# Kernel optimization log

Measured on AMD Instinct MI355X. Metric: run time of the kernel, lower is better.

## Reference

```python
import jax, jax.numpy as jnp
import numpy as np

D = 512
H = 8
FFN_H = 2048
NEG = -1.0e10


def layer_norm(x, gamma, beta, eps=1e-5):
    mu = jnp.mean(x, axis=-1, keepdims=True)
    var = jnp.var(x, axis=-1, keepdims=True)
    return (x - mu) * jax.lax.rsqrt(var + eps) * gamma + beta


def mha(x_q, x_kv, Wq, Wk, Wv, Wo, valid_lens):
    # x_q: [B,Tq,D], x_kv: [B,Tk,D]; valid_lens: [B,Tq] or [B]
    B, Tq, _ = x_q.shape
    Tk = x_kv.shape[1]
    dh = D // H
    q = (x_q @ Wq.T).reshape(B, Tq, H, dh).transpose(0, 2, 1, 3)  # [B,H,Tq,dh]
    k = (x_kv @ Wk.T).reshape(B, Tk, H, dh).transpose(0, 2, 1, 3)
    v = (x_kv @ Wv.T).reshape(B, Tk, H, dh).transpose(0, 2, 1, 3)
    scores = jnp.einsum('bhqd,bhkd->bhqk', q, k) / jnp.sqrt(jnp.float32(dh))
    pos = jnp.arange(Tk)
    if valid_lens.ndim == 1:  # [B] -> mask [B,1,1,Tk]
        mask = pos[None, None, None, :] < valid_lens[:, None, None, None]
    else:  # [B,Tq] -> mask [B,1,Tq,Tk]
        mask = pos[None, None, None, :] < valid_lens[:, None, :, None]
    scores = jnp.where(mask, scores, NEG)
    attn = jax.nn.softmax(scores, axis=-1)
    out = jnp.einsum('bhqk,bhkd->bhqd', attn, v)  # [B,H,Tq,dh]
    out = out.transpose(0, 2, 1, 3).reshape(B, Tq, D)
    return out @ Wo.T


def setup_inputs() -> dict:
    key = jax.random.key(0)
    ks = jax.random.split(key, 20)
    B, T = 32, 512
    s = 1.0 / np.sqrt(D)
    inp = {
        'X': jax.random.normal(ks[0], (B, T, D), jnp.float32),
        'enc_outputs': jax.random.normal(ks[1], (B, T, D), jnp.float32),
        'dec_valid_lens': jax.random.randint(ks[2], (B, T), 1, T + 1, jnp.int32),
        'enc_valid_lens': jax.random.randint(ks[3], (B,), 1, T + 1, jnp.int32),
    }
    names = ['Wq1', 'Wk1', 'Wv1', 'Wo1', 'Wq2', 'Wk2', 'Wv2', 'Wo2']
    for i, n in enumerate(names):
        inp[n] = jax.random.normal(ks[4 + i], (D, D), jnp.float32) * s
    inp['W1'] = jax.random.normal(ks[12], (FFN_H, D), jnp.float32) * s
    inp['b1'] = jnp.zeros((FFN_H,), jnp.float32)
    inp['W2'] = jax.random.normal(ks[13], (D, FFN_H), jnp.float32) * (1.0 / np.sqrt(FFN_H))
    inp['b2'] = jnp.zeros((D,), jnp.float32)
    for j in (1, 2, 3):
        inp[f'g{j}'] = jnp.ones((D,), jnp.float32)
        inp[f'be{j}'] = jnp.zeros((D,), jnp.float32)
    return inp


def reference(X, enc_outputs, dec_valid_lens, enc_valid_lens,
              Wq1, Wk1, Wv1, Wo1, Wq2, Wk2, Wv2, Wo2,
              W1, b1, W2, b2, g1, be1, g2, be2, g3, be3):
    # Training path: state[2][i] is None -> key_values = X. Dropout in eval mode (identity).
    X2 = mha(X, X, Wq1, Wk1, Wv1, Wo1, dec_valid_lens)            # self-attention
    Y = layer_norm(X + X2, g1, be1)                               # AddNorm1
    Y2 = mha(Y, enc_outputs, Wq2, Wk2, Wv2, Wo2, enc_valid_lens)  # cross-attention
    Z = layer_norm(Y + Y2, g2, be2)                               # AddNorm2
    F = (jax.nn.leaky_relu(Z @ W1.T + b1, 0.01)) @ W2.T + b2      # FFN (LeakyReLU slope 0.01)
    return layer_norm(Z + F, g3, be3)                             # AddNorm3
```

## Files before the change

kernel.cpp:

```cpp
#include <hip/hip_runtime.h>
#include <cstdint>
#include <cstddef>

typedef __bf16 bf16;
typedef __bf16 bf16x8 __attribute__((ext_vector_type(8)));
typedef float  f32x4  __attribute__((ext_vector_type(4)));
typedef unsigned short u16;

#define MD ((size_t)8388608)

__device__ __forceinline__ void async_copy16(const bf16* gp, bf16* lp) {
  __builtin_amdgcn_global_load_lds(
      (__attribute__((address_space(1))) void*)(gp),
      (__attribute__((address_space(3))) void*)(lp), 16, 0, 0);
}

__device__ __forceinline__ int is_f32(const u16* __restrict__ x) {
  const int e = (x[(threadIdx.x & 63) * 2] >> 7) & 0xFF;
  return __ballot(e >= 141) != 0ull;
}

struct ConvSrc { const void* p[20]; };

__global__ __launch_bounds__(256)
void convert_all(ConvSrc s, bf16* __restrict__ ws, const u16* __restrict__ xprobe)
{
  const int n[20] = {8388608, 8388608,
                     262144, 262144, 262144, 262144, 262144, 262144, 262144, 262144,
                     1048576, 2048, 1048576, 512, 512, 512, 512, 512, 512, 512};
  const unsigned int doff[20] = {
      41943040u, 50331648u,
      58720256u, 58982400u, 59244544u, 59506688u,
      59768832u, 60030976u, 60293120u, 60555264u,
      60817408u, 61865984u, 61868032u, 62916608u,
      62917120u, 62917632u, 62918144u, 62918656u, 62919168u, 62919680u};

  const int f32 = is_f32(xprobe);

  int bi = blockIdx.x;
  int idx = 0, b0 = 0;
  for (; idx < 20; ++idx) {
    const int nb = (n[idx] + 2047) >> 11;
    if (bi < b0 + nb) break;
    b0 += nb;
  }
  const int i = ((bi - b0) << 11) + threadIdx.x * 8;
  if (i >= n[idx]) return;
  bf16* dst = ws + doff[idx] + i;
  if (f32) {
    const float* sp = (const float*)s.p[idx] + i;
    f32x4 a = *(const f32x4*)sp;
    f32x4 b = *(const f32x4*)(sp + 4);
    bf16x8 o;
#pragma unroll
    for (int e = 0; e < 4; ++e) { o[e] = (bf16)a[e]; o[4 + e] = (bf16)b[e]; }
    *(bf16x8*)dst = o;
  } else {
    *(bf16x8*)dst = *(const bf16x8*)((const bf16*)s.p[idx] + i);
  }
}

template<int MODE, int BM>
__device__ __forceinline__ void gemm4p_body(
    const bf16* __restrict__ A, const bf16* __restrict__ B,
    const bf16* __restrict__ bias, bf16* __restrict__ C,
    int N, int K, int gx, int bid, int nblk, bf16* AsP, bf16* BsP)
{
  constexpr int BN = 256, T = 512, WM = 2, WN = 4;
  constexpr int WR = BM / WM;
  constexpr int MI = WR / 16;
  constexpr int NJ = 4;
  constexpr int MH = MI / 2;
  constexpr int LA = BM * 8 / T;
  constexpr int LB = 4;
  static_assert(LA == 4 || LA == 2, "schedule assumes BM in {256,128}");

  const int t    = threadIdx.x;
  const int lane = t & 63;
  const int quad = lane >> 4;
  const int l15  = lane & 15;
  const int wave = t >> 6;
  const int wm   = wave >> 2;
  const int wn   = wave & 3;

  const int chunk = nblk >> 3;
  const int lin   = (bid & 7) * chunk + (bid >> 3);
  const int m0    = (lin / gx) * BM;
  const int n0    = (lin % gx) * BN;

  const bf16* Ag = A + (size_t)m0 * K;
  const bf16* Bg = B + (size_t)n0 * K;
  const int wbase = wave << 6;

  auto stA = [&](int kt, int r, int buf) {
    const int s   = r * T + t;
    const int row = s >> 3;
    const int cg  = s & 7;
    async_copy16(Ag + (size_t)row * K + (kt << 6) + ((cg ^ (row & 7)) << 3),
                 AsP + buf * (BM * 64) + ((size_t)(r * T + wbase) << 3));
  };
  auto stB = [&](int kt, int r, int buf) {
    const int s   = r * T + t;
    const int row = s >> 3;
    const int cg  = s & 7;
    async_copy16(Bg + (size_t)row * K + (kt << 6) + ((cg ^ (row & 7)) << 3),
                 BsP + buf * (BN * 64) + ((size_t)(r * T + wbase) << 3));
  };
  auto ldfrag = [&](const bf16* base, int row, int ks) -> bf16x8 {
    return *(const bf16x8*)(base + row * 64 + ((((ks << 2) + quad) ^ (row & 7)) << 3));
  };

  const f32x4 fz = {0.f, 0.f, 0.f, 0.f};
  f32x4 acc[MI][NJ];
#pragma unroll
  for (int i = 0; i < MI; ++i)
#pragma unroll
    for (int j = 0; j < NJ; ++j) acc[i][j] = fz;

  const int nkt = K >> 6;

#pragma unroll
  for (int r = 0; r < LA; ++r) stA(0, r, 0);
#pragma unroll
  for (int r = 0; r < LB; ++r) stB(0, r, 0);
  if constexpr (LA == 4) { stA(1, 0, 1); stA(1, 2, 1); }
#pragma unroll
  for (int r = 0; r < LB; ++r) stB(1, r, 1);
  if constexpr (LA == 4) asm volatile("s_waitcnt vmcnt(6)" ::: "memory");
  else                   asm volatile("s_waitcnt vmcnt(4)" ::: "memory");
  __builtin_amdgcn_s_barrier();

  for (int j = 0; j < nkt; ++j) {
    const int cb = j & 1;
    const bf16* a_l = AsP + cb * (BM * 64);
    const bf16* b_l = BsP + cb * (BN * 64);
    const int kN = (j + 1 < nkt) ? j + 1 : nkt - 1;
    const int kF = (j + 2 < nkt) ? j + 2 : nkt - 1;

    bf16x8 bfv[NJ];
    bf16x8 af[MH];

#pragma unroll
    for (int nj = 0; nj < NJ; ++nj) bfv[nj] = ldfrag(b_l, wn * 64 + nj * 16 + l15, 0);
#pragma unroll
    for (int mi = 0; mi < MH; ++mi) af[mi] = ldfrag(a_l, wm * WR + mi * 16 + l15, 0);
    if constexpr (LA == 4) { stA(kN, 1, cb ^ 1); stA(kN, 3, cb ^ 1); }
    else                   { stA(kN, 0, cb ^ 1); stA(kN, 1, cb ^ 1); }
    __builtin_amdgcn_s_barrier();
    asm volatile("s_waitcnt lgkmcnt(0)" ::: "memory");
    __builtin_amdgcn_sched_barrier(0);
    __builtin_amdgcn_s_setprio(1);
#pragma unroll
    for (int mi = 0; mi < MH; ++mi)
#pragma unroll
      for (int nj = 0; nj < NJ; ++nj)
        acc[mi][nj] = __builtin_amdgcn_mfma_f32_16x16x32_bf16(af[mi], bfv[nj],
                                                              acc[mi][nj], 0, 0, 0);
    __builtin_amdgcn_s_setprio(0);
    __builtin_amdgcn_s_barrier();

#pragma unroll
    for (int mi = 0; mi < MH; ++mi) af[mi] = ldfrag(a_l, wm * WR + (MH + mi) * 16 + l15, 0);
    __builtin_amdgcn_s_barrier();
    asm volatile("s_waitcnt lgkmcnt(0)" ::: "memory");
    __builtin_amdgcn_sched_barrier(0);
    __builtin_amdgcn_s_setprio(1);
#pragma unroll
    for (int mi = 0; mi < MH; ++mi)
#pragma unroll
      for (int nj = 0; nj < NJ; ++nj)
        acc[MH + mi][nj] = __builtin_amdgcn_mfma_f32_16x16x32_bf16(af[mi], bfv[nj],
                                                                   acc[MH + mi][nj], 0, 0, 0);
    __builtin_amdgcn_s_setprio(0);
    __builtin_amdgcn_s_barrier();

#pragma unroll
    for (int nj = 0; nj < NJ; ++nj) bfv[nj] = ldfrag(b_l, wn * 64 + nj * 16 + l15, 1);
#pragma unroll
    for (int mi = 0; mi < MH; ++mi) af[mi] = ldfrag(a_l, wm * WR + mi * 16 + l15, 1);
    __builtin_amdgcn_s_barrier();
    asm volatile("s_waitcnt lgkmcnt(0)" ::: "memory");
    __builtin_amdgcn_sched_barrier(0);
    __builtin_amdgcn_s_setprio(1);
#pragma unroll
    for (int mi = 0; mi < MH; ++mi)
#pragma unroll
      for (int nj = 0; nj < NJ; ++nj)
        acc[mi][nj] = __builtin_amdgcn_mfma_f32_16x16x32_bf16(af[mi], bfv[nj],
                                                              acc[mi][nj], 0, 0, 0);
    __builtin_amdgcn_s_setprio(0);
    __builtin_amdgcn_s_barrier();

#pragma unroll
    for (int mi = 0; mi < MH; ++mi) af[mi] = ldfrag(a_l, wm * WR + (MH + mi) * 16 + l15, 1);
    if constexpr (LA == 4) { stA(kF, 0, cb); stA(kF, 2, cb); }
#pragma unroll
    for (int r = 0; r < LB; ++r) stB(kF, r, cb);
    __builtin_amdgcn_s_barrier();
    asm volatile("s_waitcnt lgkmcnt(0)" ::: "memory");
    __builtin_amdgcn_sched_barrier(0);
    __builtin_amdgcn_s_setprio(1);
#pragma unroll
    for (int mi = 0; mi < MH; ++mi)
#pragma unroll
      for (int nj = 0; nj < NJ; ++nj)
        acc[MH + mi][nj] = __builtin_amdgcn_mfma_f32_16x16x32_bf16(af[mi], bfv[nj],
                                                                   acc[MH + mi][nj], 0, 0, 0);
    __builtin_amdgcn_s_setprio(0);
    if constexpr (LA == 4) asm volatile("s_waitcnt vmcnt(6)" ::: "memory");
    else                   asm volatile("s_waitcnt vmcnt(4)" ::: "memory");
    __builtin_amdgcn_s_barrier();
  }

  asm volatile("s_waitcnt vmcnt(0)" ::: "memory");

#pragma unroll
  for (int mi = 0; mi < MI; ++mi) {
    const int m = m0 + wm * WR + mi * 16 + quad * 4;
#pragma unroll
    for (int nj = 0; nj < NJ; ++nj) {
      const int n = n0 + wn * 64 + nj * 16 + l15;
      float bv = 0.f;
      if (MODE >= 1) bv = (float)bias[n];
#pragma unroll
      for (int r = 0; r < 4; ++r) {
        float v = acc[mi][nj][r];
        if (MODE >= 1) v += bv;
        if (MODE == 1) v = v > 0.f ? v : 0.01f * v;
        C[(size_t)(m + r) * N + n] = (bf16)v;
      }
    }
  }
}

template<int MODE, int BM>
__global__ __launch_bounds__(512, 1)
void gemm4p(const bf16* __restrict__ A, const bf16* __restrict__ B,
            const bf16* __restrict__ bias, bf16* __restrict__ C,
            int N, int K, int gx)
{
  __shared__ __attribute__((aligned(16))) bf16 As[2 * BM * 64];
  __shared__ __attribute__((aligned(16))) bf16 Bs[2 * 256 * 64];
  gemm4p_body<MODE, BM>(A, B, bias, C, N, K, gx, blockIdx.x, gridDim.x, As, Bs);
}

__global__ __launch_bounds__(512, 1)
void gemm4p_dual(const bf16* __restrict__ A0, const bf16* __restrict__ B0,
                 bf16* __restrict__ C0,
                 const bf16* __restrict__ A1, const bf16* __restrict__ B1,
                 bf16* __restrict__ C1)
{
  __shared__ __attribute__((aligned(16))) bf16 As[2 * 256 * 64];
  __shared__ __attribute__((aligned(16))) bf16 Bs[2 * 256 * 64];
  const int bid = blockIdx.x;
  if (bid < 384)
    gemm4p_body<0, 256>(A0, B0, nullptr, C0, 1536, 512, 6, bid, 384, As, Bs);
  else
    gemm4p_body<0, 256>(A1, B1, nullptr, C1, 1024, 512, 4, bid - 384, 256, As, Bs);
}

__global__ __launch_bounds__(256, 4)
void flash_attn(const bf16* __restrict__ Qp, const bf16* __restrict__ Kp,
                const bf16* __restrict__ Vp, bf16* __restrict__ Op,
                const int* __restrict__ vlen, int per_query, int sq, int skv)
{
  __shared__ __attribute__((aligned(16))) bf16 Ks[64][72];
  __shared__ __attribute__((aligned(16))) bf16 VsT[64][72];
  __shared__ __attribute__((aligned(16))) bf16 Ps[4][32][72];
  __shared__ int vlmax_sh;

  const int t    = threadIdx.x;
  const int wave = t >> 6;
  const int lane = t & 63;
  const int quad = lane >> 4;
  const int l15  = lane & 15;
  const int bx   = blockIdx.x;
  const int qt   = bx >> 8;
  const int h    = bx & 7;
  const int b    = (bx >> 3) & 31;
  const int q0   = qt * 128 + wave * 32;

  bf16x8 qfrag[2][2];
#pragma unroll
  for (int mt = 0; mt < 2; ++mt)
#pragma unroll
    for (int ks = 0; ks < 2; ++ks)
      qfrag[mt][ks] = *(const bf16x8*)(Qp +
          (size_t)(b * 512 + q0 + mt * 16 + l15) * sq + h * 64 + ks * 32 + quad * 8);

  int vl_r[2][4];
  int myvl = 1;
#pragma unroll
  for (int mt = 0; mt < 2; ++mt)
#pragma unroll
    for (int r = 0; r < 4; ++r) {
      const int q = q0 + mt * 16 + quad * 4 + r;
      const int v = per_query ? vlen[b * 512 + q] : vlen[b];
      vl_r[mt][r] = v;
      myvl = v > myvl ? v : myvl;
    }

  if (t == 0) vlmax_sh = 1;
  __syncthreads();
#pragma unroll
  for (int off = 1; off < 64; off <<= 1) {
    const int o = __shfl_xor(myvl, off);
    myvl = o > myvl ? o : myvl;
  }
  if (lane == 0) atomicMax(&vlmax_sh, myvl);
  __syncthreads();
  const int ktiles = (vlmax_sh + 63) >> 6;

  const f32x4 fz = {0.f, 0.f, 0.f, 0.f};
  float l_part[2][4] = {{0.f,0.f,0.f,0.f},{0.f,0.f,0.f,0.f}};
  f32x4 o_acc[2][4];
#pragma unroll
  for (int mt = 0; mt < 2; ++mt)
#pragma unroll
    for (int nt = 0; nt < 4; ++nt) o_acc[mt][nt] = fz;

  for (int kt = 0; kt < ktiles; ++kt) {
    const int k0 = kt * 64;
    __syncthreads();
    {
      const int r0 = t >> 3;
      const int c0 = (t & 7) * 8;
      const bf16* g = Kp + (size_t)(b * 512 + k0 + r0) * skv + h * 64 + c0;
      *(bf16x8*)&Ks[r0][c0]      = *(const bf16x8*)g;
      *(bf16x8*)&Ks[r0 + 32][c0] = *(const bf16x8*)(g + (size_t)32 * skv);
    }
    {
      const bf16* g = Vp + (size_t)(b * 512 + k0 + wave * 16) * skv + h * 64 + lane;
      bf16x8 lo, hi;
#pragma unroll
      for (int kk = 0; kk < 8; ++kk) lo[kk] = g[(size_t)kk * skv];
#pragma unroll
      for (int kk = 0; kk < 8; ++kk) hi[kk] = g[(size_t)(kk + 8) * skv];
      *(bf16x8*)&VsT[lane][wave * 16]     = lo;
      *(bf16x8*)&VsT[lane][wave * 16 + 8] = hi;
    }
    __syncthreads();

    f32x4 s[2][4];
#pragma unroll
    for (int mt = 0; mt < 2; ++mt)
#pragma unroll
      for (int nt = 0; nt < 4; ++nt) s[mt][nt] = fz;
#pragma unroll
    for (int ks = 0; ks < 2; ++ks)
#pragma unroll
      for (int nt = 0; nt < 4; ++nt) {
        const bf16x8 bk = *(const bf16x8*)&Ks[nt * 16 + l15][ks * 32 + quad * 8];
        s[0][nt] = __builtin_amdgcn_mfma_f32_16x16x32_bf16(qfrag[0][ks], bk, s[0][nt], 0, 0, 0);
        s[1][nt] = __builtin_amdgcn_mfma_f32_16x16x32_bf16(qfrag[1][ks], bk, s[1][nt], 0, 0, 0);
      }

#pragma unroll
    for (int mt = 0; mt < 2; ++mt)
#pragma unroll
      for (int nt = 0; nt < 4; ++nt) {
        const int k_abs = k0 + nt * 16 + l15;
#pragma unroll
        for (int r = 0; r < 4; ++r) {
          const float p = (k_abs < vl_r[mt][r]) ? __expf(s[mt][nt][r] * 0.125f) : 0.f;
          l_part[mt][r] += p;
          Ps[wave][mt * 16 + quad * 4 + r][nt * 16 + l15] = (bf16)p;
        }
      }

#pragma unroll
    for (int ks = 0; ks < 2; ++ks) {
      const bf16x8 ap0 = *(const bf16x8*)&Ps[wave][l15][ks * 32 + quad * 8];
      const bf16x8 ap1 = *(const bf16x8*)&Ps[wave][16 + l15][ks * 32 + quad * 8];
#pragma unroll
      for (int nt = 0; nt < 4; ++nt) {
        const bf16x8 bv = *(const bf16x8*)&VsT[nt * 16 + l15][ks * 32 + quad * 8];
        o_acc[0][nt] = __builtin_amdgcn_mfma_f32_16x16x32_bf16(ap0, bv, o_acc[0][nt], 0, 0, 0);
        o_acc[1][nt] = __builtin_amdgcn_mfma_f32_16x16x32_bf16(ap1, bv, o_acc[1][nt], 0, 0, 0);
      }
    }
  }

#pragma unroll
  for (int mt = 0; mt < 2; ++mt)
#pragma unroll
    for (int r = 0; r < 4; ++r) {
      float l = l_part[mt][r];
#pragma unroll
      for (int off = 1; off < 16; off <<= 1)
        l += __shfl_xor(l, off);
      const float inv_l = (l > 0.f) ? (1.f / l) : 0.f;
      const int q = q0 + mt * 16 + quad * 4 + r;
#pragma unroll
      for (int nt = 0; nt < 4; ++nt)
        Op[(size_t)(b * 512 + q) * 512 + h * 64 + nt * 16 + l15] =
            (bf16)(o_acc[mt][nt][r] * inv_l);
    }
}

__global__ __launch_bounds__(256)
void add_layernorm(const bf16* X, const bf16* R,
                   const bf16* __restrict__ gamma, const bf16* __restrict__ beta,
                   bf16* Out)
{
  const int t    = threadIdx.x;
  const int wave = t >> 6;
  const int lane = t & 63;
  const size_t row  = (size_t)blockIdx.x * 4 + wave;
  const size_t base = row * 512 + lane * 8;

  bf16x8 xv = *(const bf16x8*)(X + base);
  bf16x8 rv = *(const bf16x8*)(R + base);
  float v[8];
  float sum = 0.f, ss = 0.f;
#pragma unroll
  for (int i = 0; i < 8; ++i) {
    v[i] = (float)xv[i] + (float)rv[i];
    sum += v[i];
    ss  += v[i] * v[i];
  }
#pragma unroll
  for (int off = 1; off < 64; off <<= 1) {
    sum += __shfl_xor(sum, off);
    ss  += __shfl_xor(ss, off);
  }
  const float mean = sum * (1.f / 512.f);
  const float var  = ss * (1.f / 512.f) - mean * mean;
  const float rstd = rsqrtf(var + 1e-5f);

  bf16x8 gv = *(const bf16x8*)(gamma + lane * 8);
  bf16x8 bv = *(const bf16x8*)(beta + lane * 8);
  bf16x8 ov;
#pragma unroll
  for (int i = 0; i < 8; ++i)
    ov[i] = (bf16)(((v[i] - mean) * rstd) * (float)gv[i] + (float)bv[i]);
  *(bf16x8*)(Out + base) = ov;
}

__global__ __launch_bounds__(256)
void add_layernorm_out(const bf16* X, const bf16* R,
                       const bf16* __restrict__ gamma, const bf16* __restrict__ beta,
                       void* Out, const u16* __restrict__ xprobe)
{
  const int t    = threadIdx.x;
  const int wave = t >> 6;
  const int lane = t & 63;
  const size_t row  = (size_t)blockIdx.x * 4 + wave;
  const size_t base = row * 512 + lane * 8;

  const int f32 = is_f32(xprobe);

  bf16x8 xv = *(const bf16x8*)(X + base);
  bf16x8 rv = *(const bf16x8*)(R + base);
  float v[8];
  float sum = 0.f, ss = 0.f;
#pragma unroll
  for (int i = 0; i < 8; ++i) {
    v[i] = (float)xv[i] + (float)rv[i];
    sum += v[i];
    ss  += v[i] * v[i];
  }
#pragma unroll
  for (int off = 1; off < 64; off <<= 1) {
    sum += __shfl_xor(sum, off);
    ss  += __shfl_xor(ss, off);
  }
  const float mean = sum * (1.f / 512.f);
  const float var  = ss * (1.f / 512.f) - mean * mean;
  const float rstd = rsqrtf(var + 1e-5f);

  bf16x8 gv = *(const bf16x8*)(gamma + lane * 8);
  bf16x8 bv = *(const bf16x8*)(beta + lane * 8);
  float o[8];
#pragma unroll
  for (int i = 0; i < 8; ++i)
    o[i] = ((v[i] - mean) * rstd) * (float)gv[i] + (float)bv[i];

  if (f32) {
    float* op = (float*)Out + base;
    f32x4 o0 = {o[0], o[1], o[2], o[3]};
    f32x4 o1 = {o[4], o[5], o[6], o[7]};
    *(f32x4*)op       = o0;
    *(f32x4*)(op + 4) = o1;
  } else {
    bf16x8 ov;
#pragma unroll
    for (int i = 0; i < 8; ++i) ov[i] = (bf16)o[i];
    *(bf16x8*)((bf16*)Out + base) = ov;
  }
}

extern "C" void kernel_launch(void* const* d_in, const int* in_sizes, int n_in,
                              void* d_out, int out_size, void* d_ws, size_t ws_size,
                              hipStream_t stream)
{
  (void)in_sizes; (void)n_in; (void)out_size; (void)ws_size;

  const int* dvl = (const int*)d_in[2];
  const int* evl = (const int*)d_in[3];
  const u16* xprobe = (const u16*)d_in[0];

  bf16* ws = (bf16*)d_ws;
  bf16* S0 = ws;
  bf16* S1 = ws + 1 * MD;
  bf16* S2 = ws + 2 * MD;
  bf16* S3 = ws + 3 * MD;
  bf16* S4 = ws + 4 * MD;
  bf16* Xb = ws + 5 * MD;
  bf16* Eb = ws + 6 * MD;
  bf16* W  = ws + 7 * MD;
  const bf16 *Wq1 = W,
             *Wo1 = W + 786432,   *Wq2 = W + 1048576, *Wk2 = W + 1310720,
             *Wo2 = W + 1835008,
             *W1  = W + 2097152,  *b1  = W + 3145728,
             *W2  = W + 3147776,  *b2  = W + 4196352,
             *g1  = W + 4196864,  *be1 = W + 4197376,
             *g2  = W + 4197888,  *be2 = W + 4198400,
             *g3  = W + 4198912,  *be3 = W + 4199424;

  ConvSrc cs;
  cs.p[0] = d_in[0];  cs.p[1] = d_in[1];
  for (int k = 0; k < 12; ++k) cs.p[2 + k] = d_in[4 + k];
  for (int k = 0; k < 6; ++k)  cs.p[14 + k] = d_in[16 + k];
  convert_all<<<dim3(10248), dim3(256), 0, stream>>>(cs, ws, xprobe);

  dim3 blk256(256);
  dim3 blk512(512);

  gemm4p_dual<<<dim3(640), blk512, 0, stream>>>(Xb, Wq1, S0, Eb, Wk2, S3);

  flash_attn<<<dim3(1024), blk256, 0, stream>>>(S0, S0 + 512, S0 + 1024, Eb, dvl, 1, 1536, 1536);
  gemm4p<0,128><<<dim3(256), blk512, 0, stream>>>(Eb, Wo1, nullptr, S0, 512, 512, 2);
  add_layernorm<<<dim3(4096), blk256, 0, stream>>>(Xb, S0, g1, be1, S1);

  gemm4p<0,128><<<dim3(256), blk512, 0, stream>>>(S1, Wq2, nullptr, S2, 512, 512, 2);
  flash_attn<<<dim3(1024), blk256, 0, stream>>>(S2, S3, S3 + 512, S0, evl, 0, 512, 1024);
  gemm4p<0,128><<<dim3(256), blk512, 0, stream>>>(S0, Wo2, nullptr, S2, 512, 512, 2);
  add_layernorm<<<dim3(4096), blk256, 0, stream>>>(S1, S2, g2, be2, S4);

  gemm4p<1,256><<<dim3(512), blk512, 0, stream>>>(S4, W1, b1, S0, 2048, 512, 8);
  gemm4p<2,128><<<dim3(256), blk512, 0, stream>>>(S0, W2, b2, Xb, 512, 2048, 2);
  add_layernorm_out<<<dim3(4096), blk256, 0, stream>>>(S4, Xb, g3, be3, d_out, xprobe);
}
```

Before: 465.1 us.

## Fuse add-layernorm into GEMM epilogues via atomic row statistics and folded gamma

Removes the two intermediate add_layernorm kernels. GEMM epilogues now add the residual and accumulate per-row sum and sum-of-squares into global stats with atomics. The next GEMM applies the normalization algebraically, using W·gamma folded into the weights during conversion plus precomputed column sums and W·beta terms. This saves full-tensor read/write passes and launches, but adds atomics and an un-normalized intermediate whose one-pass variance formula can lose precision in bf16.

New measurement: 506.3 us. 8.8% more time.

```diff
diff --git a/kernel.cpp b/kernel.cpp
--- a/kernel.cpp
+++ b/kernel.cpp
@@ -8,6 +8,7 @@
 typedef unsigned short u16;
 
 #define MD ((size_t)8388608)
+#define STATS_OFF ((size_t)62920192)
 
 __device__ __forceinline__ void async_copy16(const bf16* gp, bf16* lp) {
   __builtin_amdgcn_global_load_lds(
@@ -20,11 +21,51 @@
   return __ballot(e >= 141) != 0ull;
 }
 
+__device__ __forceinline__ float elemf(const void* p, int i, int f32) {
+  return f32 ? ((const float*)p)[i] : (float)((const bf16*)p)[i];
+}
+
 struct ConvSrc { const void* p[20]; };
 
 __global__ __launch_bounds__(256)
 void convert_all(ConvSrc s, bf16* __restrict__ ws, const u16* __restrict__ xprobe)
 {
+  const int bi = blockIdx.x;
+  if (bi >= 10248) {
+    float* ST = (float*)(ws + STATS_OFF);
+    const int j = bi - 10248;
+    if (j < 24) {
+      const f32x4 z = {0.f, 0.f, 0.f, 0.f};
+      const int base = j * 4096 + threadIdx.x * 16;
+#pragma unroll
+      for (int q = 0; q < 4; ++q) *(f32x4*)(ST + base + q * 4) = z;
+      return;
+    }
+    const int f32 = is_f32(xprobe);
+    const int lane = threadIdx.x & 63;
+    const int nidx = (j - 24) * 4 + (threadIdx.x >> 6);
+    const void *Wp, *gp, *bp; int row; float *cs, *bw;
+    if (nidx < 512) { Wp = s.p[6];  gp = s.p[14]; bp = s.p[15];
+                      row = nidx;       cs = ST + 98304; bw = ST + 98816; }
+    else            { Wp = s.p[10]; gp = s.p[16]; bp = s.p[17];
+                      row = nidx - 512; cs = ST + 99328; bw = ST + 101376; }
+    float sg = 0.f, sb = 0.f;
+#pragma unroll
+    for (int e = 0; e < 8; ++e) {
+      const int k = lane * 8 + e;
+      const float wv = elemf(Wp, row * 512 + k, f32);
+      sg += wv * elemf(gp, k, f32);
+      sb += wv * elemf(bp, k, f32);
+    }
+#pragma unroll
+    for (int off = 1; off < 64; off <<= 1) {
+      sg += __shfl_xor(sg, off);
+      sb += __shfl_xor(sb, off);
+    }
+    if (lane == 0) { cs[row] = sg; bw[row] = sb; }
+    return;
+  }
+
   const int n[20] = {8388608, 8388608,
                      262144, 262144, 262144, 262144, 262144, 262144, 262144, 262144,
                      1048576, 2048, 1048576, 512, 512, 512, 512, 512, 512, 512};
@@ -37,34 +78,57 @@
 
   const int f32 = is_f32(xprobe);
 
-  int bi = blockIdx.x;
-  int idx = 0, b0 = 0;
+  int b = bi, idx = 0, b0 = 0;
   for (; idx < 20; ++idx) {
     const int nb = (n[idx] + 2047) >> 11;
-    if (bi < b0 + nb) break;
+    if (b < b0 + nb) break;
     b0 += nb;
   }
-  const int i = ((bi - b0) << 11) + threadIdx.x * 8;
+  const int i = ((b - b0) << 11) + threadIdx.x * 8;
   if (i >= n[idx]) return;
   bf16* dst = ws + doff[idx] + i;
+
+  float vals[8];
   if (f32) {
     const float* sp = (const float*)s.p[idx] + i;
     f32x4 a = *(const f32x4*)sp;
-    f32x4 b = *(const f32x4*)(sp + 4);
-    bf16x8 o;
-#pragma unroll
-    for (int e = 0; e < 4; ++e) { o[e] = (bf16)a[e]; o[4 + e] = (bf16)b[e]; }
-    *(bf16x8*)dst = o;
+    f32x4 c = *(const f32x4*)(sp + 4);
+#pragma unroll
+    for (int e = 0; e < 4; ++e) { vals[e] = a[e]; vals[4 + e] = c[e]; }
   } else {
-    *(bf16x8*)dst = *(const bf16x8*)((const bf16*)s.p[idx] + i);
-  }
-}
+    bf16x8 raw = *(const bf16x8*)((const bf16*)s.p[idx] + i);
+#pragma unroll
+    for (int e = 0; e < 8; ++e) vals[e] = (float)raw[e];
+  }
+  if (idx == 6) {
+#pragma unroll
+    for (int e = 0; e < 8; ++e) vals[e] *= elemf(s.p[14], (i + e) & 511, f32);
+  } else if (idx == 10) {
+#pragma unroll
+    for (int e = 0; e < 8; ++e) vals[e] *= elemf(s.p[16], (i + e) & 511, f32);
+  }
+  bf16x8 o;
+#pragma unroll
+  for (int e = 0; e < 8; ++e) o[e] = (bf16)vals[e];
+  *(bf16x8*)dst = o;
+}
+
+struct Epi {
+  const bf16*  res;
+  const float* st_in;
+  float*       st_out;
+  const float* cs;
+  const float* bw;
+  const bf16*  gam;
+  const bf16*  bet;
+  const bf16*  bias;
+};
 
 template<int MODE, int BM>
 __device__ __forceinline__ void gemm4p_body(
     const bf16* __restrict__ A, const bf16* __restrict__ B,
-    const bf16* __restrict__ bias, bf16* __restrict__ C,
-    int N, int K, int gx, int bid, int nblk, bf16* AsP, bf16* BsP)
+    bf16* __restrict__ C, int N, int K, int gx, int bid, int nblk,
+    bf16* AsP, bf16* BsP, const Epi& ep)
 {
   constexpr int BN = 256, T = 512, WM = 2, WN = 4;
   constexpr int WR = BM / WM;
@@ -217,17 +281,60 @@
 #pragma unroll
   for (int mi = 0; mi < MI; ++mi) {
     const int m = m0 + wm * WR + mi * 16 + quad * 4;
+    float mu[4], rs[4];
+    if constexpr (MODE >= 4) {
+#pragma unroll
+      for (int r = 0; r < 4; ++r) {
+        const float sv = ep.st_in[2 * (m + r)];
+        const float qv = ep.st_in[2 * (m + r) + 1];
+        const float mm = sv * (1.f / 512.f);
+        const float va = qv * (1.f / 512.f) - mm * mm;
+        mu[r] = mm; rs[r] = rsqrtf(va + 1e-5f);
+      }
+    }
+    float rsum[4] = {0.f, 0.f, 0.f, 0.f}, rss[4] = {0.f, 0.f, 0.f, 0.f};
 #pragma unroll
     for (int nj = 0; nj < NJ; ++nj) {
       const int n = n0 + wn * 64 + nj * 16 + l15;
-      float bv = 0.f;
-      if (MODE >= 1) bv = (float)bias[n];
+      float csn = 0.f, bwn = 0.f, gan = 0.f, ben = 0.f, bin = 0.f;
+      if constexpr (MODE == 4 || MODE == 6) { csn = ep.cs[n]; bwn = ep.bw[n]; }
+      if constexpr (MODE == 5 || MODE == 7) { gan = (float)ep.gam[n]; ben = (float)ep.bet[n]; }
+      if constexpr (MODE == 6 || MODE == 7) bin = (float)ep.bias[n];
 #pragma unroll
       for (int r = 0; r < 4; ++r) {
         float v = acc[mi][nj][r];
-        if (MODE >= 1) v += bv;
-        if (MODE == 1) v = v > 0.f ? v : 0.01f * v;
+        if constexpr (MODE == 3)
+          v += (float)ep.res[(size_t)(m + r) * N + n];
+        if constexpr (MODE == 4)
+          v = rs[r] * (v - mu[r] * csn) + bwn;
+        if constexpr (MODE == 5)
+          v += rs[r] * ((float)ep.res[(size_t)(m + r) * N + n] - mu[r]) * gan + ben;
+        if constexpr (MODE == 6) {
+          v = rs[r] * (v - mu[r] * csn) + bwn + bin;
+          v = v > 0.f ? v : 0.01f * v;
+        }
+        if constexpr (MODE == 7)
+          v += bin + rs[r] * ((float)ep.res[(size_t)(m + r) * N + n] - mu[r]) * gan + ben;
+        if constexpr (MODE == 3 || MODE == 5 || MODE == 7) {
+          rsum[r] += v; rss[r] += v * v;
+        }
         C[(size_t)(m + r) * N + n] = (bf16)v;
+      }
+    }
+    if constexpr (MODE == 3 || MODE == 5 || MODE == 7) {
+#pragma unroll
+      for (int r = 0; r < 4; ++r)
+#pragma unroll
+        for (int off = 1; off < 16; off <<= 1) {
+          rsum[r] += __shfl_xor(rsum[r], off);
+          rss[r]  += __shfl_xor(rss[r], off);
+        }
+      if (l15 == 0) {
+#pragma unroll
+        for (int r = 0; r < 4; ++r) {
+          atomicAdd(&ep.st_out[2 * (m + r)],     rsum[r]);
+          atomicAdd(&ep.st_out[2 * (m + r) + 1], rss[r]);
+        }
       }
     }
   }
@@ -236,12 +343,11 @@
 template<int MODE, int BM>
 __global__ __launch_bounds__(512, 1)
 void gemm4p(const bf16* __restrict__ A, const bf16* __restrict__ B,
-            const bf16* __restrict__ bias, bf16* __restrict__ C,
-            int N, int K, int gx)
+            bf16* __restrict__ C, int N, int K, int gx, Epi ep)
 {
   __shared__ __attribute__((aligned(16))) bf16 As[2 * BM * 64];
   __shared__ __attribute__((aligned(16))) bf16 Bs[2 * 256 * 64];
-  gemm4p_body<MODE, BM>(A, B, bias, C, N, K, gx, blockIdx.x, gridDim.x, As, Bs);
+  gemm4p_body<MODE, BM>(A, B, C, N, K, gx, blockIdx.x, gridDim.x, As, Bs, ep);
 }
 
 __global__ __launch_bounds__(512, 1)
@@ -252,11 +358,12 @@
 {
   __shared__ __attribute__((aligned(16))) bf16 As[2 * 256 * 64];
   __shared__ __attribute__((aligned(16))) bf16 Bs[2 * 256 * 64];
+  Epi e{};
   const int bid = blockIdx.x;
   if (bid < 384)
-    gemm4p_body<0, 256>(A0, B0, nullptr, C0, 1536, 512, 6, bid, 384, As, Bs);
+    gemm4p_body<0, 256>(A0, B0, C0, 1536, 512, 6, bid, 384, As, Bs, e);
   else
-    gemm4p_body<0, 256>(A1, B1, nullptr, C1, 1024, 512, 4, bid - 384, 256, As, Bs);
+    gemm4p_body<0, 256>(A1, B1, C1, 1024, 512, 4, bid - 384, 256, As, Bs, e);
 }
 
 __global__ __launch_bounds__(256, 4)
@@ -399,9 +506,9 @@
 }
 
 __global__ __launch_bounds__(256)
-void add_layernorm(const bf16* X, const bf16* R,
-                   const bf16* __restrict__ gamma, const bf16* __restrict__ beta,
-                   bf16* Out)
+void ln_final(const bf16* __restrict__ R, const float* __restrict__ st,
+              const bf16* __restrict__ gamma, const bf16* __restrict__ beta,
+              void* Out, const u16* __restrict__ xprobe)
 {
   const int t    = threadIdx.x;
   const int wave = t >> 6;
@@ -409,72 +516,20 @@
   const size_t row  = (size_t)blockIdx.x * 4 + wave;
   const size_t base = row * 512 + lane * 8;
 
-  bf16x8 xv = *(const bf16x8*)(X + base);
-  bf16x8 rv = *(const bf16x8*)(R + base);
-  float v[8];
-  float sum = 0.f, ss = 0.f;
-#pragma unroll
-  for (int i = 0; i < 8; ++i) {
-    v[i] = (float)xv[i] + (float)rv[i];
-    sum += v[i];
-    ss  += v[i] * v[i];
-  }
-#pragma unroll
-  for (int off = 1; off < 64; off <<= 1) {
-    sum += __shfl_xor(sum, off);
-    ss  += __shfl_xor(ss, off);
-  }
-  const float mean = sum * (1.f / 512.f);
-  const float var  = ss * (1.f / 512.f) - mean * mean;
+  const int f32 = is_f32(xprobe);
+
+  const float sv = st[2 * row], qv = st[2 * row + 1];
+  const float mean = sv * (1.f / 512.f);
+  const float var  = qv * (1.f / 512.f) - mean * mean;
   const float rstd = rsqrtf(var + 1e-5f);
 
-  bf16x8 gv = *(const bf16x8*)(gamma + lane * 8);
-  bf16x8 bv = *(const bf16x8*)(beta + lane * 8);
-  bf16x8 ov;
-#pragma unroll
-  for (int i = 0; i < 8; ++i)
-    ov[i] = (bf16)(((v[i] - mean) * rstd) * (float)gv[i] + (float)bv[i]);
-  *(bf16x8*)(Out + base) = ov;
-}
-
-__global__ __launch_bounds__(256)
-void add_layernorm_out(const bf16* X, const bf16* R,
-                       const bf16* __restrict__ gamma, const bf16* __restrict__ beta,
-                       void* Out, const u16* __restrict__ xprobe)
-{
-  const int t    = threadIdx.x;
-  const int wave = t >> 6;
-  const int lane = t & 63;
-  const size_t row  = (size_t)blockIdx.x * 4 + wave;
-  const size_t base = row * 512 + lane * 8;
-
-  const int f32 = is_f32(xprobe);
-
-  bf16x8 xv = *(const bf16x8*)(X + base);
-  bf16x8 rv = *(const bf16x8*)(R + base);
-  float v[8];
-  float sum = 0.f, ss = 0.f;
-#pragma unroll
-  for (int i = 0; i < 8; ++i) {
-    v[i] = (float)xv[i] + (float)rv[i];
-    sum += v[i];
-    ss  += v[i] * v[i];
-  }
-#pragma unroll
-  for (int off = 1; off < 64; off <<= 1) {
-    sum += __shfl_xor(sum, off);
-    ss  += __shfl_xor(ss, off);
-  }
-  const float mean = sum * (1.f / 512.f);
-  const float var  = ss * (1.f / 512.f) - mean * mean;
-  const float rstd = rsqrtf(var + 1e-5f);
-
+  bf16x8 xv = *(const bf16x8*)(R + base);
   bf16x8 gv = *(const bf16x8*)(gamma + lane * 8);
   bf16x8 bv = *(const bf16x8*)(beta + lane * 8);
   float o[8];
 #pragma unroll
   for (int i = 0; i < 8; ++i)
-    o[i] = ((v[i] - mean) * rstd) * (float)gv[i] + (float)bv[i];
+    o[i] = ((float)xv[i] - mean) * rstd * (float)gv[i] + (float)bv[i];
 
   if (f32) {
     float* op = (float*)Out + base;
@@ -505,24 +560,32 @@
   bf16* S1 = ws + 1 * MD;
   bf16* S2 = ws + 2 * MD;
   bf16* S3 = ws + 3 * MD;
-  bf16* S4 = ws + 4 * MD;
   bf16* Xb = ws + 5 * MD;
   bf16* Eb = ws + 6 * MD;
   bf16* W  = ws + 7 * MD;
   const bf16 *Wq1 = W,
              *Wo1 = W + 786432,   *Wq2 = W + 1048576, *Wk2 = W + 1310720,
              *Wo2 = W + 1835008,
-             *W1  = W + 2097152,  *b1  = W + 3145728,
+             *W1  = W + 2097152,
              *W2  = W + 3147776,  *b2  = W + 4196352,
+             *b1  = W + 3145728,
              *g1  = W + 4196864,  *be1 = W + 4197376,
              *g2  = W + 4197888,  *be2 = W + 4198400,
              *g3  = W + 4198912,  *be3 = W + 4199424;
+
+  float* ST1 = (float*)(ws + STATS_OFF);
+  float* ST2 = ST1 + 32768;
+  float* ST3 = ST1 + 65536;
+  const float* CSQ = ST1 + 98304;
+  const float* BWQ = ST1 + 98816;
+  const float* CSW = ST1 + 99328;
+  const float* BWW = ST1 + 101376;
 
   ConvSrc cs;
   cs.p[0] = d_in[0];  cs.p[1] = d_in[1];
   for (int k = 0; k < 12; ++k) cs.p[2 + k] = d_in[4 + k];
   for (int k = 0; k < 6; ++k)  cs.p[14 + k] = d_in[16 + k];
-  convert_all<<<dim3(10248), dim3(256), 0, stream>>>(cs, ws, xprobe);
+  convert_all<<<dim3(10912), dim3(256), 0, stream>>>(cs, ws, xprobe);
 
   dim3 blk256(256);
   dim3 blk512(512);
@@ -530,15 +593,19 @@
   gemm4p_dual<<<dim3(640), blk512, 0, stream>>>(Xb, Wq1, S0, Eb, Wk2, S3);
 
   flash_attn<<<dim3(1024), blk256, 0, stream>>>(S0, S0 + 512, S0 + 1024, Eb, dvl, 1, 1536, 1536);
-  gemm4p<0,128><<<dim3(256), blk512, 0, stream>>>(Eb, Wo1, nullptr, S0, 512, 512, 2);
-  add_layernorm<<<dim3(4096), blk256, 0, stream>>>(Xb, S0, g1, be1, S1);
-
-  gemm4p<0,128><<<dim3(256), blk512, 0, stream>>>(S1, Wq2, nullptr, S2, 512, 512, 2);
-  flash_attn<<<dim3(1024), blk256, 0, stream>>>(S2, S3, S3 + 512, S0, evl, 0, 512, 1024);
-  gemm4p<0,128><<<dim3(256), blk512, 0, stream>>>(S0, Wo2, nullptr, S2, 512, 512, 2);
-  add_layernorm<<<dim3(4096), blk256, 0, stream>>>(S1, S2, g2, be2, S4);
-
-  gemm4p<1,256><<<dim3(512), blk512, 0, stream>>>(S4, W1, b1, S0, 2048, 512, 8);
-  gemm4p<2,128><<<dim3(256), blk512, 0, stream>>>(S0, W2, b2, Xb, 512, 2048, 2);
-  add_layernorm_out<<<dim3(4096), blk256, 0, stream>>>(S4, Xb, g3, be3, d_out, xprobe);
-}
+  { Epi e{}; e.res = Xb; e.st_out = ST1;
+    gemm4p<3,128><<<dim3(256), blk512, 0, stream>>>(Eb, Wo1, S0, 512, 512, 2, e); }
+
+  { Epi e{}; e.st_in = ST1; e.cs = CSQ; e.bw = BWQ;
+    gemm4p<4,128><<<dim3(256), blk512, 0, stream>>>(S0, Wq2, S1, 512, 512, 2, e); }
+  flash_attn<<<dim3(1024), blk256, 0, stream>>>(S1, S3, S3 + 512, S2, evl, 0, 512, 1024);
+  { Epi e{}; e.res = S0; e.st_in = ST1; e.gam = g1; e.bet = be1; e.st_out = ST2;
+    gemm4p<5,128><<<dim3(256), blk512, 0, stream>>>(S2, Wo2, S1, 512, 512, 2, e); }
+
+  { Epi e{}; e.st_in = ST2; e.cs = CSW; e.bw = BWW; e.bias = b1;
+    gemm4p<6,256><<<dim3(512), blk512, 0, stream>>>(S1, W1, S2, 2048, 512, 8, e); }
+  { Epi e{}; e.res = S1; e.st_in = ST2; e.gam = g2; e.bet = be2; e.bias = b2; e.st_out = ST3;
+    gemm4p<7,128><<<dim3(256), blk512, 0, stream>>>(S2, W2, S0, 512, 2048, 2, e); }
+
+  ln_final<<<dim3(4096), blk256, 0, stream>>>(S0, ST3, g3, be3, d_out, xprobe);
+}
```
